# Kernel optimization log

Hardware: AMD Instinct MI355X
Metric: run time of the kernel (lower is better)

Reference implementation:

```python
import jax, jax.numpy as jnp
import numpy as np

NEG_SLOPE = 0.1  # LReLu_neg_slope
WEIGHT_INIT_STD = 1.0
N_GEN, N_LOAD, N_END = 25000, 25000, 25000
N_NODES = 100000
N_EDGES = 1600000
H = 128
N_HIDDEN_LAYERS = 3  # N_GCN_layers - 1


def _lin_w(key, n_in, n_out):
    # torch init: normal(std = weight_init_std / in_channels); stored as (in, out) for jax
    return jax.random.normal(key, (n_in, n_out), dtype=jnp.float32) * (WEIGHT_INIT_STD / n_in)


def setup_inputs() -> dict:
    key = jax.random.key(0)
    ks = jax.random.split(key, 24)
    inp = {
        "x_gen": jax.random.normal(ks[0], (N_GEN, 3), dtype=jnp.float32),
        "x_load": jax.random.normal(ks[1], (N_LOAD, 3), dtype=jnp.float32),
        "x_or": jax.random.normal(ks[2], (N_END, 6), dtype=jnp.float32),
        "x_ex": jax.random.normal(ks[3], (N_END, 6), dtype=jnp.float32),
        "edge_index": jax.random.randint(ks[4], (2, N_EDGES), 0, N_NODES, dtype=jnp.int64)
        if jax.config.jax_enable_x64 else jax.random.randint(ks[4], (2, N_EDGES), 0, N_NODES, dtype=jnp.int32),
        "object_ptv": jnp.arange(N_NODES, dtype=jnp.int32),
    }
    # per-type embedding MLPs (2 Linear layers each)
    inp["Wg1"], inp["bg1"] = _lin_w(ks[5], 3, H), jnp.zeros((H,), jnp.float32)
    inp["Wg2"], inp["bg2"] = _lin_w(ks[6], H, H), jnp.zeros((H,), jnp.float32)
    inp["Wld1"], inp["bld1"] = _lin_w(ks[7], 3, H), jnp.zeros((H,), jnp.float32)
    inp["Wld2"], inp["bld2"] = _lin_w(ks[8], H, H), jnp.zeros((H,), jnp.float32)
    inp["Wor1"], inp["bor1"] = _lin_w(ks[9], 6, H), jnp.zeros((H,), jnp.float32)
    inp["Wor2"], inp["bor2"] = _lin_w(ks[10], H, H), jnp.zeros((H,), jnp.float32)
    inp["Wex1"], inp["bex1"] = _lin_w(ks[11], 6, H), jnp.zeros((H,), jnp.float32)
    inp["Wex2"], inp["bex2"] = _lin_w(ks[12], H, H), jnp.zeros((H,), jnp.float32)
    # hidden SAGEConv layers (stacked): lin_l (neighbor, with bias) + lin_r (root, no bias)
    inp["Wl_h"] = jnp.stack([_lin_w(ks[13 + i], H, H) for i in range(N_HIDDEN_LAYERS)])
    inp["bl_h"] = jnp.zeros((N_HIDDEN_LAYERS, H), jnp.float32)
    inp["Wr_h"] = jnp.stack([_lin_w(ks[16 + i], H, H) for i in range(N_HIDDEN_LAYERS)])
    # output SAGEConv layer -> 1 unit
    inp["Wl_o"], inp["bl_o"] = _lin_w(ks[19], H, 1), jnp.zeros((1,), jnp.float32)
    inp["Wr_o"] = _lin_w(ks[20], H, 1)
    return inp


def _lrelu(x):
    return jax.nn.leaky_relu(x, NEG_SLOPE)


def _embed(x, W1, b1, W2, b2):
    return _lrelu(_lrelu(x @ W1 + b1) @ W2 + b2)


def reference(x_gen, x_load, x_or, x_ex, edge_index, object_ptv,
              Wg1, bg1, Wg2, bg2, Wld1, bld1, Wld2, bld2,
              Wor1, bor1, Wor2, bor2, Wex1, bex1, Wex2, bex2,
              Wl_h, bl_h, Wr_h, Wl_o, bl_o, Wr_o):
    x = jnp.concatenate([
        _embed(x_gen, Wg1, bg1, Wg2, bg2),
        _embed(x_load, Wld1, bld1, Wld2, bld2),
        _embed(x_or, Wor1, bor1, Wor2, bor2),
        _embed(x_ex, Wex1, bex1, Wex2, bex2),
    ], axis=0)
    x = x[object_ptv]                      # [N, H] in topology-vector order
    src, dst = edge_index[0], edge_index[1]
    n = x.shape[0]
    deg = jax.ops.segment_sum(jnp.ones_like(src, dtype=x.dtype), dst, num_segments=n)
    inv_deg = (1.0 / jnp.maximum(deg, 1.0))[:, None]

    def sage(h, Wl, bl, Wr):
        # SAGEConv(aggr='mean', root_weight=True): lin_l(mean_j h_j) + bias + lin_r(h_i)
        agg = jax.ops.segment_sum(h[src], dst, num_segments=n) * inv_deg
        return agg @ Wl + bl + h @ Wr

    for i in range(Wl_h.shape[0]):
        x = _lrelu(sage(x, Wl_h[i], bl_h[i], Wr_h[i]))
    return jax.nn.sigmoid(sage(x, Wl_o, bl_o, Wr_o))  # [N, 1]
```

## Files before the change

kernel.cpp:

```cpp
#include <hip/hip_runtime.h>
#include <hip/hip_bf16.h>
#include <hip/hip_fp16.h>
#include <math.h>

#define HD 128
#define NPB 512
#define CAP 16384
#define SCHUNK 4096
#define ALCSR 768

typedef __attribute__((ext_vector_type(8))) short  bf16x8;
typedef __attribute__((ext_vector_type(4))) float  f32x4;
typedef __attribute__((ext_vector_type(2))) _Float16 h16x2;

__device__ __forceinline__ float lrelu(float v) { return v > 0.0f ? v : 0.1f * v; }

__device__ __forceinline__ unsigned short f2bf(float f) {
  union { float f; unsigned u; } c; c.f = f;
  unsigned u = c.u + 0x7fffu + ((c.u >> 16) & 1u);
  return (unsigned short)(u >> 16);
}
__device__ __forceinline__ float bf2f(unsigned short u) {
  return __uint_as_float((unsigned)u << 16);
}
__device__ __forceinline__ unsigned char f2e5m2(float f) {
  unsigned short h = __half_as_ushort(__float2half(f));
  h = (unsigned short)(h + 0x7f + ((h >> 8) & 1));
  return (unsigned char)(h >> 8);
}

__global__ __launch_bounds__(256)
void embed1_kernel(const float* __restrict__ xg, const float* __restrict__ xl,
                   const float* __restrict__ xo, const float* __restrict__ xe,
                   const float* __restrict__ Wg, const float* __restrict__ bg,
                   const float* __restrict__ Wl, const float* __restrict__ bl,
                   const float* __restrict__ Wo, const float* __restrict__ bo,
                   const float* __restrict__ We, const float* __restrict__ be,
                   unsigned short* __restrict__ h1, int4 padCum, int4 realCnt) {
  int p = blockIdx.x * 2 + (threadIdx.x >> 7);
  if (p >= padCum.w) return;
  int j = threadIdx.x & 127;
  int typ = (p < padCum.x) ? 0 : (p < padCum.y) ? 1 : (p < padCum.z) ? 2 : 3;
  int padStart = (typ == 0) ? 0 : (typ == 1) ? padCum.x : (typ == 2) ? padCum.y : padCum.z;
  int cnt = (typ == 0) ? realCnt.x : (typ == 1) ? realCnt.y : (typ == 2) ? realCnt.z : realCnt.w;
  int loc = p - padStart;
  if (loc >= cnt) return;
  const float *x, *W, *bb; int IN;
  if (typ == 0)      { x = xg; W = Wg; bb = bg; IN = 3; }
  else if (typ == 1) { x = xl; W = Wl; bb = bl; IN = 3; }
  else if (typ == 2) { x = xo; W = Wo; bb = bo; IN = 6; }
  else               { x = xe; W = We; bb = be; IN = 6; }
  float acc = bb[j];
  for (int k = 0; k < IN; k++) acc += x[(size_t)loc * IN + k] * W[k * HD + j];
  h1[(size_t)p * HD + j] = f2bf(lrelu(acc));
}

__global__ __launch_bounds__(256)
void wprep_all_kernel(const float* __restrict__ Wg2, const float* __restrict__ Wld2,
                      const float* __restrict__ Wor2, const float* __restrict__ Wex2,
                      const float* __restrict__ Wl_h, const float* __restrict__ Wr_h,
                      unsigned short* __restrict__ Wp,
                      const int* __restrict__ ptv, int* __restrict__ inv,
                      int* __restrict__ gcnt, int n) {
  int tid = blockIdx.x * 256 + threadIdx.x;
  if (tid < 256) gcnt[tid] = 0;
  if (tid < n) inv[ptv[tid]] = tid;
  int m = tid >> 14;
  int i = tid & 16383;
  const float* src; unsigned short* dst;
  switch (m) {
    case 0: src = Wg2;  dst = Wp;             break;
    case 1: src = Wld2; dst = Wp + 16384;     break;
    case 2: src = Wor2; dst = Wp + 2 * 16384; break;
    case 3: src = Wex2; dst = Wp + 3 * 16384; break;
    default: {
      int mm = m - 4; int l = mm >> 1; int isR = mm & 1;
      src = (isR ? Wr_h : Wl_h) + (size_t)l * 16384;
      dst = Wp + 4 * 16384 + (size_t)l * 32768 + (isR ? 16384 : 0);
    }
  }
  int k = i >> 7, j = i & 127;
  int ks = k >> 5, g = (k >> 3) & 3, b = k & 7;
  dst[((ks * 128 + j) * 4 + g) * 8 + b] = f2bf(src[i]);
}

__global__ __launch_bounds__(256)
void mfma_embed2_kernel(const unsigned short* __restrict__ h1,
                        const unsigned short* __restrict__ Wp,
                        const float* __restrict__ b_g, const float* __restrict__ b_ld,
                        const float* __restrict__ b_or, const float* __restrict__ b_ex,
                        const int* __restrict__ inv, unsigned short* __restrict__ out,
                        int4 padCum, int4 realStart, int4 realCnt) {
  const int t = threadIdx.x, w = t >> 6, l = t & 63;
  const int lr = l & 15, lg = l >> 4;
  const int prow0 = blockIdx.x * 64 + w * 16;
  int typ = (prow0 < padCum.x) ? 0 : (prow0 < padCum.y) ? 1 : (prow0 < padCum.z) ? 2 : 3;
  int padStart = (typ == 0) ? 0 : (typ == 1) ? padCum.x : (typ == 2) ? padCum.y : padCum.z;
  int rStart = (typ == 0) ? realStart.x : (typ == 1) ? realStart.y : (typ == 2) ? realStart.z : realStart.w;
  int cnt = (typ == 0) ? realCnt.x : (typ == 1) ? realCnt.y : (typ == 2) ? realCnt.z : realCnt.w;
  const float* bias = (typ == 0) ? b_g : (typ == 1) ? b_ld : (typ == 2) ? b_or : b_ex;

  int raLoc = prow0 + lr - padStart; if (raLoc >= cnt) raLoc = cnt - 1;
  const unsigned short* abase = h1 + (size_t)(padStart + raLoc) * HD + 8 * lg;
  const unsigned short* wbase = Wp + (size_t)typ * 16384 + lr * 32 + lg * 8;

  f32x4 acc[8];
  #pragma unroll
  for (int cb = 0; cb < 8; cb++) {
    float bv = bias[cb * 16 + lr];
    acc[cb] = (f32x4){bv, bv, bv, bv};
  }
  #pragma unroll
  for (int ks = 0; ks < 4; ks++) {
    bf16x8 af = *(const bf16x8*)(abase + ks * 32);
    #pragma unroll
    for (int cb = 0; cb < 8; cb++) {
      bf16x8 bfv = *(const bf16x8*)(wbase + (size_t)(ks * 128 + cb * 16) * 32);
      acc[cb] = __builtin_amdgcn_mfma_f32_16x16x32_bf16(af, bfv, acc[cb], 0, 0, 0);
    }
  }
  int tgt[4];
  #pragma unroll
  for (int r = 0; r < 4; r++) {
    int locRow = prow0 + lg * 4 + r - padStart;
    tgt[r] = (locRow < cnt) ? inv[rStart + locRow] : -1;
  }
  #pragma unroll
  for (int cb = 0; cb < 8; cb++) {
    #pragma unroll
    for (int r = 0; r < 4; r++) {
      if (tgt[r] >= 0)
        out[(size_t)tgt[r] * HD + cb * 16 + lr] = f2bf(lrelu(acc[cb][r]));
    }
  }
}

__global__ __launch_bounds__(256)
void bf2f8_kernel(const unsigned short* __restrict__ in, unsigned char* __restrict__ out, int n8) {
  int idx = blockIdx.x * 256 + threadIdx.x;
  if (idx >= n8) return;
  uint4 v = *(const uint4*)(in + (size_t)idx * 8);
  unsigned char b0 = f2e5m2(__uint_as_float(v.x << 16));
  unsigned char b1 = f2e5m2(__uint_as_float(v.x & 0xffff0000u));
  unsigned char b2 = f2e5m2(__uint_as_float(v.y << 16));
  unsigned char b3 = f2e5m2(__uint_as_float(v.y & 0xffff0000u));
  unsigned char b4 = f2e5m2(__uint_as_float(v.z << 16));
  unsigned char b5 = f2e5m2(__uint_as_float(v.z & 0xffff0000u));
  unsigned char b6 = f2e5m2(__uint_as_float(v.w << 16));
  unsigned char b7 = f2e5m2(__uint_as_float(v.w & 0xffff0000u));
  uint2 o;
  o.x = (unsigned)b0 | ((unsigned)b1 << 8) | ((unsigned)b2 << 16) | ((unsigned)b3 << 24);
  o.y = (unsigned)b4 | ((unsigned)b5 << 8) | ((unsigned)b6 << 16) | ((unsigned)b7 << 24);
  *(uint2*)(out + (size_t)idx * 8) = o;
}

__global__ __launch_bounds__(256)
void bucket_scatter_kernel(const int* __restrict__ esrc, const int* __restrict__ edst,
                           int* __restrict__ gcnt, int* __restrict__ ebuf, int nE) {
  __shared__ int cnt[256];
  __shared__ int cur[256];
  const int t = threadIdx.x;
  const int c0 = blockIdx.x * SCHUNK;
  int s_arr[16], d_arr[16];
  cnt[t] = 0;
  __syncthreads();
  #pragma unroll
  for (int k = 0; k < 16; k++) {
    int idx = c0 + k * 256 + t;
    if (idx < nE) {
      s_arr[k] = esrc[idx];
      int d = edst[idx];
      d_arr[k] = d;
      atomicAdd(&cnt[d >> 9], 1);
    } else d_arr[k] = -1;
  }
  __syncthreads();
  if (cnt[t] > 0) cur[t] = atomicAdd(&gcnt[t], cnt[t]);
  __syncthreads();
  #pragma unroll
  for (int k = 0; k < 16; k++) {
    if (d_arr[k] >= 0) {
      int b = d_arr[k] >> 9;
      int p = atomicAdd(&cur[b], 1);
      ebuf[(size_t)b * CAP + p] = (s_arr[k] << 9) | (d_arr[k] & 511);
    }
  }
}

__device__ __forceinline__ int wave_incl_scan(int v) {
  int lane = threadIdx.x & 63;
  #pragma unroll
  for (int d = 1; d < 64; d <<= 1) {
    int tv = __shfl_up(v, d, 64);
    if (lane >= d) v += tv;
  }
  return v;
}

__global__ __launch_bounds__(256)
void bucket_build_kernel(const int* __restrict__ ebuf, const int* __restrict__ gcnt,
                         int* __restrict__ csr, int* __restrict__ offs,
                         int* __restrict__ deg, float* __restrict__ inv_deg, int n) {
  __shared__ int hist[512];
  __shared__ int offl[512];
  __shared__ int wsum[4];
  const int b = blockIdx.x, t = threadIdx.x;
  const int cnt = gcnt[b];
  const size_t ebase = (size_t)b * CAP;
  hist[t] = 0; hist[t + 256] = 0;
  __syncthreads();
  for (int i = t; i < cnt; i += 256) {
    int e = ebuf[ebase + i];
    atomicAdd(&hist[e & 511], 1);
  }
  __syncthreads();
  int a0 = hist[2 * t], a1 = hist[2 * t + 1];
  int s = a0 + a1;
  int incl = wave_incl_scan(s);
  int wid = t >> 6;
  if ((t & 63) == 63) wsum[wid] = incl;
  __syncthreads();
  int wbase = 0;
  for (int w_ = 0; w_ < wid; w_++) wbase += wsum[w_];
  int excl = wbase + incl - s;
  offl[2 * t] = excl;
  offl[2 * t + 1] = excl + a0;
  __syncthreads();
  const int d0 = b << 9;
  for (int i = t; i < 512; i += 256) {
    int g = d0 + i;
    if (g < n) {
      offs[g] = b * CAP + offl[i];
      int dg = hist[i];
      deg[g] = dg;
      inv_deg[g] = 1.0f / fmaxf((float)dg, 1.0f);
    }
  }
  __syncthreads();
  for (int i = t; i < cnt; i += 256) {
    int e = ebuf[ebase + i];
    int p = atomicAdd(&offl[e & 511], 1);
    csr[ebase + p] = ((unsigned)e) >> 9;
  }
}

template<bool EMIT_Z>
__global__ __launch_bounds__(256)
void sage_fused_kernel(const unsigned short* __restrict__ x, const unsigned char* __restrict__ xf8,
                       const int* __restrict__ csr,
                       const int* __restrict__ offs, const int* __restrict__ deg,
                       const float* __restrict__ inv_deg,
                       const unsigned short* __restrict__ Wp, const float* __restrict__ bias,
                       unsigned short* __restrict__ out, unsigned char* __restrict__ outf8,
                       const float* __restrict__ wl, const float* __restrict__ wr,
                       float* __restrict__ zl, float* __restrict__ zr, int n) {
  __shared__ int lcsr[ALCSR];
  __shared__ __align__(16) unsigned short lagg[16][136];
  __shared__ float zpart[2][4][16];
  const int t = threadIdx.x;
  const int node0 = blockIdx.x * 16;
  int last = node0 + 15; if (last >= n) last = n - 1;
  const int s_begin = offs[node0];
  const int total = offs[last] + deg[last] - s_begin;
  const bool useLds = (total <= ALCSR);
  if (useLds) {
    for (int k = t; k < total; k += 256) lcsr[k] = csr[s_begin + k];
  }
  __syncthreads();

  const int w = t >> 6, l = t & 63;
  {
    const int g = l >> 4, j = l & 15;
    const int node = node0 + w * 4 + g;
    if (node < n) {
      const unsigned char* xj = xf8 + 8 * j;
      const int lb = offs[node] - s_begin;
      const int d = deg[node];
      h16x2 a0[4], a1[4];
      #pragma unroll
      for (int k = 0; k < 4; k++) {
        a0[k] = (h16x2){(_Float16)0, (_Float16)0};
        a1[k] = (h16x2){(_Float16)0, (_Float16)0};
      }
      auto acc8 = [](h16x2* A, uint2 v) {
        unsigned p0 = __builtin_amdgcn_perm(0u, v.x, 0x01040004u);
        unsigned p1 = __builtin_amdgcn_perm(0u, v.x, 0x03040204u);
        unsigned p2 = __builtin_amdgcn_perm(0u, v.y, 0x01040004u);
        unsigned p3 = __builtin_amdgcn_perm(0u, v.y, 0x03040204u);
        A[0] += __builtin_bit_cast(h16x2, p0);
        A[1] += __builtin_bit_cast(h16x2, p1);
        A[2] += __builtin_bit_cast(h16x2, p2);
        A[3] += __builtin_bit_cast(h16x2, p3);
      };
      int i = 0;
      if (useLds) {
        for (; i + 3 < d; i += 4) {
          int e0 = lcsr[lb + i], e1 = lcsr[lb + i + 1];
          int e2 = lcsr[lb + i + 2], e3 = lcsr[lb + i + 3];
          uint2 v0 = *(const uint2*)(xj + (size_t)e0 * HD);
          uint2 v1 = *(const uint2*)(xj + (size_t)e1 * HD);
          uint2 v2 = *(const uint2*)(xj + (size_t)e2 * HD);
          uint2 v3 = *(const uint2*)(xj + (size_t)e3 * HD);
          acc8(a0, v0); acc8(a1, v1); acc8(a0, v2); acc8(a1, v3);
        }
        if (i + 1 < d) {
          int e0 = lcsr[lb + i], e1 = lcsr[lb + i + 1];
          uint2 v0 = *(const uint2*)(xj + (size_t)e0 * HD);
          uint2 v1 = *(const uint2*)(xj + (size_t)e1 * HD);
          acc8(a0, v0); acc8(a1, v1);
          i += 2;
        }
        if (i < d) {
          int e0 = lcsr[lb + i];
          acc8(a0, *(const uint2*)(xj + (size_t)e0 * HD));
        }
      } else {
        const int* gcsr = csr + s_begin + lb;
        for (; i + 3 < d; i += 4) {
          int e0 = gcsr[i], e1 = gcsr[i + 1], e2 = gcsr[i + 2], e3 = gcsr[i + 3];
          uint2 v0 = *(const uint2*)(xj + (size_t)e0 * HD);
          uint2 v1 = *(const uint2*)(xj + (size_t)e1 * HD);
          uint2 v2 = *(const uint2*)(xj + (size_t)e2 * HD);
          uint2 v3 = *(const uint2*)(xj + (size_t)e3 * HD);
          acc8(a0, v0); acc8(a1, v1); acc8(a0, v2); acc8(a1, v3);
        }
        if (i + 1 < d) {
          int e0 = gcsr[i], e1 = gcsr[i + 1];
          uint2 v0 = *(const uint2*)(xj + (size_t)e0 * HD);
          uint2 v1 = *(const uint2*)(xj + (size_t)e1 * HD);
          acc8(a0, v0); acc8(a1, v1);
          i += 2;
        }
        if (i < d) {
          int e0 = gcsr[i];
          acc8(a0, *(const uint2*)(xj + (size_t)e0 * HD));
        }
      }
      const float id = inv_deg[node];
      uint4 o;
      unsigned* op = (unsigned*)&o;
      #pragma unroll
      for (int k = 0; k < 4; k++) {
        float lo = ((float)a0[k][0] + (float)a1[k][0]) * id;
        float hi = ((float)a0[k][1] + (float)a1[k][1]) * id;
        op[k] = (unsigned)f2bf(lo) | ((unsigned)f2bf(hi) << 16);
      }
      *(uint4*)&lagg[w * 4 + g][j * 8] = o;
    } else {
      *(uint4*)&lagg[w * 4 + g][j * 8] = make_uint4(0, 0, 0, 0);
    }
  }
  __syncthreads();

  const int lr = l & 15, lg = l >> 4;
  int ra = node0 + lr; if (ra >= n) ra = n - 1;
  const unsigned short* wbase = Wp + (size_t)lr * 32 + (size_t)lg * 8;
  const unsigned short* rbase = x + (size_t)ra * HD + 8 * lg;

  f32x4 acc[2];
  #pragma unroll
  for (int c = 0; c < 2; c++) {
    float bv = bias[(2 * w + c) * 16 + lr];
    acc[c] = (f32x4){bv, bv, bv, bv};
  }
  #pragma unroll
  for (int ks = 0; ks < 4; ks++) {
    bf16x8 af = *(const bf16x8*)&lagg[lr][lg * 8 + ks * 32];
    #pragma unroll
    for (int c = 0; c < 2; c++) {
      int cb = 2 * w + c;
      bf16x8 bfv = *(const bf16x8*)(wbase + (size_t)(ks * 128 + cb * 16) * 32);
      acc[c] = __builtin_amdgcn_mfma_f32_16x16x32_bf16(af, bfv, acc[c], 0, 0, 0);
    }
  }
  #pragma unroll
  for (int ks = 0; ks < 4; ks++) {
    bf16x8 af = *(const bf16x8*)(rbase + ks * 32);
    #pragma unroll
    for (int c = 0; c < 2; c++) {
      int cb = 2 * w + c;
      bf16x8 bfv = *(const bf16x8*)(wbase + (size_t)((4 + ks) * 128 + cb * 16) * 32);
      acc[c] = __builtin_amdgcn_mfma_f32_16x16x32_bf16(af, bfv, acc[c], 0, 0, 0);
    }
  }

  if constexpr (!EMIT_Z) {
    #pragma unroll
    for (int c = 0; c < 2; c++) {
      int cb = 2 * w + c;
      #pragma unroll
      for (int r = 0; r < 4; r++) {
        int node = node0 + lg * 4 + r;
        if (node < n) {
          float val = lrelu(acc[c][r]);
          out[(size_t)node * HD + cb * 16 + lr] = f2bf(val);
          outf8[(size_t)node * HD + cb * 16 + lr] = f2e5m2(val);
        }
      }
    }
  } else {
    float vl[4] = {0.f, 0.f, 0.f, 0.f}, vr[4] = {0.f, 0.f, 0.f, 0.f};
    #pragma unroll
    for (int c = 0; c < 2; c++) {
      int cb = 2 * w + c;
      float wlv = wl[cb * 16 + lr];
      float wrv = wr[cb * 16 + lr];
      #pragma unroll
      for (int r = 0; r < 4; r++) {
        float x3 = lrelu(acc[c][r]);
        vl[r] += x3 * wlv;
        vr[r] += x3 * wrv;
      }
    }
    #pragma unroll
    for (int r = 0; r < 4; r++) {
      #pragma unroll
      for (int d = 1; d < 16; d <<= 1) {
        vl[r] += __shfl_xor(vl[r], d, 64);
        vr[r] += __shfl_xor(vr[r], d, 64);
      }
    }
    if (lr == 0) {
      #pragma unroll
      for (int r = 0; r < 4; r++) {
        zpart[0][w][lg * 4 + r] = vl[r];
        zpart[1][w][lg * 4 + r] = vr[r];
      }
    }
    __syncthreads();
    if (t < 16) {
      int node = node0 + t;
      if (node < n) {
        zl[node] = zpart[0][0][t] + zpart[0][1][t] + zpart[0][2][t] + zpart[0][3][t];
        zr[node] = zpart[1][0][t] + zpart[1][1][t] + zpart[1][2][t] + zpart[1][3][t];
      }
    }
  }
}

__global__ __launch_bounds__(256)
void zfinal_kernel(const float* __restrict__ zl, const float* __restrict__ zr,
                   const int* __restrict__ csr, const int* __restrict__ offs,
                   const int* __restrict__ deg, const float* __restrict__ inv_deg,
                   const float* __restrict__ bl, float* __restrict__ out, int n) {
  int i = blockIdx.x * 256 + threadIdx.x;
  if (i >= n) return;
  int s0 = offs[i], d = deg[i];
  float a = 0.f;
  #pragma unroll 4
  for (int e = 0; e < d; e++) a += zl[csr[s0 + e]];
  float s = a * inv_deg[i] + bl[0] + zr[i];
  out[i] = 1.0f / (1.0f + expf(-s));
}

extern "C" void kernel_launch(void* const* d_in, const int* in_sizes, int n_in,
                              void* d_out, int out_size, void* d_ws, size_t ws_size,
                              hipStream_t stream) {
  const float* x_gen  = (const float*)d_in[0];
  const float* x_load = (const float*)d_in[1];
  const float* x_or   = (const float*)d_in[2];
  const float* x_ex   = (const float*)d_in[3];
  const int*   edge   = (const int*)d_in[4];
  const int*   ptv    = (const int*)d_in[5];
  const float* Wg1  = (const float*)d_in[6],  *bg1  = (const float*)d_in[7];
  const float* Wg2  = (const float*)d_in[8],  *bg2  = (const float*)d_in[9];
  const float* Wld1 = (const float*)d_in[10], *bld1 = (const float*)d_in[11];
  const float* Wld2 = (const float*)d_in[12], *bld2 = (const float*)d_in[13];
  const float* Wor1 = (const float*)d_in[14], *bor1 = (const float*)d_in[15];
  const float* Wor2 = (const float*)d_in[16], *bor2 = (const float*)d_in[17];
  const float* Wex1 = (const float*)d_in[18], *bex1 = (const float*)d_in[19];
  const float* Wex2 = (const float*)d_in[20], *bex2 = (const float*)d_in[21];
  const float* Wl_h = (const float*)d_in[22], *bl_h = (const float*)d_in[23];
  const float* Wr_h = (const float*)d_in[24];
  const float* Wl_o = (const float*)d_in[25], *bl_o = (const float*)d_in[26];
  const float* Wr_o = (const float*)d_in[27];

  const int n_gen  = in_sizes[0] / 3;
  const int n_load = in_sizes[1] / 3;
  const int n_or   = in_sizes[2] / 6;
  const int n_ex   = in_sizes[3] / 6;
  const int nE     = in_sizes[4] / 2;
  const int N      = in_sizes[5];
  const int* esrc = edge;
  const int* edst = edge + nE;

  const int np0 = ((n_gen  + 63) / 64) * 64;
  const int np1 = ((n_load + 63) / 64) * 64;
  const int np2 = ((n_or   + 63) / 64) * 64;
  const int np3 = ((n_ex   + 63) / 64) * 64;
  const int NP  = np0 + np1 + np2 + np3;
  const int4 padCum    = make_int4(np0, np0 + np1, np0 + np1 + np2, NP);
  const int4 realStart = make_int4(0, n_gen, n_gen + n_load, n_gen + n_load + n_or);
  const int4 realCnt   = make_int4(n_gen, n_load, n_or, n_ex);

  const int NB = (N + NPB - 1) / NPB;

  size_t NPel = (size_t)NP * HD;
  size_t nel  = (size_t)N * HD;
  unsigned short* b0 = (unsigned short*)d_ws;
  unsigned short* b1 = b0 + NPel;
  unsigned short* b3 = b1 + nel;
  int*  gcnt = (int*)(b3 + nel);
  int*  ebuf = gcnt + 256;
  int*  csr  = ebuf + (size_t)NB * CAP;
  int*  offs = csr + (size_t)NB * CAP;
  int*  deg  = offs + N;
  float* inv_deg = (float*)(deg + N);
  float* zl = inv_deg + N;
  float* zr = zl + N;
  int*  invp = (int*)(zr + N);
  uintptr_t wp_addr = ((uintptr_t)(invp + N) + 15) & ~(uintptr_t)15;
  unsigned short* Wp = (unsigned short*)wp_addr;
  uintptr_t f8_addr = ((uintptr_t)(Wp + 4 * 16384 + 3 * 32768) + 15) & ~(uintptr_t)15;
  unsigned char* f8a = (unsigned char*)f8_addr;
  unsigned char* f8b = f8a + nel;

  wprep_all_kernel<<<640, 256, 0, stream>>>(Wg2, Wld2, Wor2, Wex2, Wl_h, Wr_h, Wp,
                                            ptv, invp, gcnt, N);

  embed1_kernel<<<NP / 2, 256, 0, stream>>>(x_gen, x_load, x_or, x_ex,
                                            Wg1, bg1, Wld1, bld1, Wor1, bor1, Wex1, bex1,
                                            b0, padCum, realCnt);
  mfma_embed2_kernel<<<NP / 64, 256, 0, stream>>>(b0, Wp, bg2, bld2, bor2, bex2,
                                                  invp, b1, padCum, realStart, realCnt);
  bf2f8_kernel<<<(N * 16 + 255) / 256, 256, 0, stream>>>(b1, f8a, N * 16);

  bucket_scatter_kernel<<<(nE + SCHUNK - 1) / SCHUNK, 256, 0, stream>>>(esrc, edst, gcnt, ebuf, nE);
  bucket_build_kernel<<<NB, 256, 0, stream>>>(ebuf, gcnt, csr, offs, deg, inv_deg, N);

  const int fGrid = (N + 15) / 16;
  const unsigned short* WpC = Wp + 4 * 16384;
  unsigned short* xbf = b1;  unsigned char* xf8 = f8a;
  unsigned short* nbf = b3;  unsigned char* nf8 = f8b;
  for (int l = 0; l < 2; l++) {
    sage_fused_kernel<false><<<fGrid, 256, 0, stream>>>(
        xbf, xf8, csr, offs, deg, inv_deg, WpC + (size_t)l * 32768,
        bl_h + (size_t)l * HD, nbf, nf8, nullptr, nullptr, nullptr, nullptr, N);
    unsigned short* tb = xbf; xbf = nbf; nbf = tb;
    unsigned char*  tf = xf8; xf8 = nf8; nf8 = tf;
  }
  sage_fused_kernel<true><<<fGrid, 256, 0, stream>>>(
      xbf, xf8, csr, offs, deg, inv_deg, WpC + 2 * 32768,
      bl_h + 2 * HD, nullptr, nullptr, Wl_o, Wr_o, zl, zr, N);

  zfinal_kernel<<<(N + 255) / 256, 256, 0, stream>>>(zl, zr, csr, offs, deg, inv_deg,
                                                     bl_o, (float*)d_out, N);
}
```

Baseline: 319.6 us.

## Fuse fp8 conversion into embed epilogue and stage CSR build through LDS

The embed GEMM epilogue now writes the e5m2 copy directly, which removes the separate bf16-to-fp8 kernel and its extra pass over the activations. The bucket scatter first sorts each chunk's edges locally in shared memory, then writes them out contiguously per bucket, so global stores coalesce better. The CSR build permutes edges in an LDS buffer and writes the CSR sequentially when the bucket fits, falling back to global scatter otherwise. The costs are larger shared-memory footprints, which may reduce occupancy, and a binary search per element during the scatter write-out.

```diff
diff --git a/kernel.cpp b/kernel.cpp
--- a/kernel.cpp
+++ b/kernel.cpp
@@ -8,6 +8,7 @@
 #define CAP 16384
 #define SCHUNK 4096
 #define ALCSR 768
+#define LCAP 9216
 
 typedef __attribute__((ext_vector_type(8))) short  bf16x8;
 typedef __attribute__((ext_vector_type(4))) float  f32x4;
@@ -90,6 +91,7 @@
                         const float* __restrict__ b_g, const float* __restrict__ b_ld,
                         const float* __restrict__ b_or, const float* __restrict__ b_ex,
                         const int* __restrict__ inv, unsigned short* __restrict__ out,
+                        unsigned char* __restrict__ outf8,
                         int4 padCum, int4 realStart, int4 realCnt) {
   const int t = threadIdx.x, w = t >> 6, l = t & 63;
   const int lr = l & 15, lg = l >> 4;
@@ -129,36 +131,34 @@
   for (int cb = 0; cb < 8; cb++) {
     #pragma unroll
     for (int r = 0; r < 4; r++) {
-      if (tgt[r] >= 0)
-        out[(size_t)tgt[r] * HD + cb * 16 + lr] = f2bf(lrelu(acc[cb][r]));
-    }
-  }
-}
-
-__global__ __launch_bounds__(256)
-void bf2f8_kernel(const unsigned short* __restrict__ in, unsigned char* __restrict__ out, int n8) {
-  int idx = blockIdx.x * 256 + threadIdx.x;
-  if (idx >= n8) return;
-  uint4 v = *(const uint4*)(in + (size_t)idx * 8);
-  unsigned char b0 = f2e5m2(__uint_as_float(v.x << 16));
-  unsigned char b1 = f2e5m2(__uint_as_float(v.x & 0xffff0000u));
-  unsigned char b2 = f2e5m2(__uint_as_float(v.y << 16));
-  unsigned char b3 = f2e5m2(__uint_as_float(v.y & 0xffff0000u));
-  unsigned char b4 = f2e5m2(__uint_as_float(v.z << 16));
-  unsigned char b5 = f2e5m2(__uint_as_float(v.z & 0xffff0000u));
-  unsigned char b6 = f2e5m2(__uint_as_float(v.w << 16));
-  unsigned char b7 = f2e5m2(__uint_as_float(v.w & 0xffff0000u));
-  uint2 o;
-  o.x = (unsigned)b0 | ((unsigned)b1 << 8) | ((unsigned)b2 << 16) | ((unsigned)b3 << 24);
-  o.y = (unsigned)b4 | ((unsigned)b5 << 8) | ((unsigned)b6 << 16) | ((unsigned)b7 << 24);
-  *(uint2*)(out + (size_t)idx * 8) = o;
+      if (tgt[r] >= 0) {
+        float val = lrelu(acc[cb][r]);
+        out[(size_t)tgt[r] * HD + cb * 16 + lr] = f2bf(val);
+        outf8[(size_t)tgt[r] * HD + cb * 16 + lr] = f2e5m2(val);
+      }
+    }
+  }
+}
+
+__device__ __forceinline__ int wave_incl_scan(int v) {
+  int lane = threadIdx.x & 63;
+  #pragma unroll
+  for (int d = 1; d < 64; d <<= 1) {
+    int tv = __shfl_up(v, d, 64);
+    if (lane >= d) v += tv;
+  }
+  return v;
 }
 
 __global__ __launch_bounds__(256)
 void bucket_scatter_kernel(const int* __restrict__ esrc, const int* __restrict__ edst,
                            int* __restrict__ gcnt, int* __restrict__ ebuf, int nE) {
   __shared__ int cnt[256];
+  __shared__ int loff[257];
+  __shared__ int gbase[256];
   __shared__ int cur[256];
+  __shared__ int wsum[4];
+  __shared__ int sbuf[SCHUNK];
   const int t = threadIdx.x;
   const int c0 = blockIdx.x * SCHUNK;
   int s_arr[16], d_arr[16];
@@ -175,26 +175,37 @@
     } else d_arr[k] = -1;
   }
   __syncthreads();
-  if (cnt[t] > 0) cur[t] = atomicAdd(&gcnt[t], cnt[t]);
+  int v = cnt[t];
+  int incl = wave_incl_scan(v);
+  int wid = t >> 6;
+  if ((t & 63) == 63) wsum[wid] = incl;
+  if (v > 0) gbase[t] = atomicAdd(&gcnt[t], v);
+  __syncthreads();
+  int add = 0;
+  for (int w_ = 0; w_ < wid; w_++) add += wsum[w_];
+  int excl = add + incl - v;
+  loff[t] = excl;
+  cur[t] = excl;
+  if (t == 255) loff[256] = excl + v;
   __syncthreads();
   #pragma unroll
   for (int k = 0; k < 16; k++) {
     if (d_arr[k] >= 0) {
       int b = d_arr[k] >> 9;
       int p = atomicAdd(&cur[b], 1);
-      ebuf[(size_t)b * CAP + p] = (s_arr[k] << 9) | (d_arr[k] & 511);
-    }
-  }
-}
-
-__device__ __forceinline__ int wave_incl_scan(int v) {
-  int lane = threadIdx.x & 63;
-  #pragma unroll
-  for (int d = 1; d < 64; d <<= 1) {
-    int tv = __shfl_up(v, d, 64);
-    if (lane >= d) v += tv;
-  }
-  return v;
+      sbuf[p] = (s_arr[k] << 9) | (d_arr[k] & 511);
+    }
+  }
+  __syncthreads();
+  const int totalc = loff[256];
+  for (int k = t; k < totalc; k += 256) {
+    int lo = 0, hi = 255;
+    while (lo < hi) {
+      int mid = (lo + hi + 1) >> 1;
+      if (loff[mid] <= k) lo = mid; else hi = mid - 1;
+    }
+    ebuf[(size_t)lo * CAP + gbase[lo] + (k - loff[lo])] = sbuf[k];
+  }
 }
 
 __global__ __launch_bounds__(256)
@@ -203,7 +214,9 @@
                          int* __restrict__ deg, float* __restrict__ inv_deg, int n) {
   __shared__ int hist[512];
   __shared__ int offl[512];
+  __shared__ int curl[512];
   __shared__ int wsum[4];
+  __shared__ int lbuf[LCAP];
   const int b = blockIdx.x, t = threadIdx.x;
   const int cnt = gcnt[b];
   const size_t ebase = (size_t)b * CAP;
@@ -220,11 +233,11 @@
   int wid = t >> 6;
   if ((t & 63) == 63) wsum[wid] = incl;
   __syncthreads();
-  int wbase = 0;
-  for (int w_ = 0; w_ < wid; w_++) wbase += wsum[w_];
-  int excl = wbase + incl - s;
-  offl[2 * t] = excl;
-  offl[2 * t + 1] = excl + a0;
+  int add = 0;
+  for (int w_ = 0; w_ < wid; w_++) add += wsum[w_];
+  int excl = add + incl - s;
+  offl[2 * t] = excl;     offl[2 * t + 1] = excl + a0;
+  curl[2 * t] = excl;     curl[2 * t + 1] = excl + a0;
   __syncthreads();
   const int d0 = b << 9;
   for (int i = t; i < 512; i += 256) {
@@ -237,10 +250,20 @@
     }
   }
   __syncthreads();
-  for (int i = t; i < cnt; i += 256) {
-    int e = ebuf[ebase + i];
-    int p = atomicAdd(&offl[e & 511], 1);
-    csr[ebase + p] = ((unsigned)e) >> 9;
+  if (cnt <= LCAP) {
+    for (int i = t; i < cnt; i += 256) {
+      int e = ebuf[ebase + i];
+      int p = atomicAdd(&curl[e & 511], 1);
+      lbuf[p] = ((unsigned)e) >> 9;
+    }
+    __syncthreads();
+    for (int i = t; i < cnt; i += 256) csr[ebase + i] = lbuf[i];
+  } else {
+    for (int i = t; i < cnt; i += 256) {
+      int e = ebuf[ebase + i];
+      int p = atomicAdd(&curl[e & 511], 1);
+      csr[ebase + p] = ((unsigned)e) >> 9;
+    }
   }
 }
 
@@ -522,8 +545,7 @@
                                             Wg1, bg1, Wld1, bld1, Wor1, bor1, Wex1, bex1,
                                             b0, padCum, realCnt);
   mfma_embed2_kernel<<<NP / 64, 256, 0, stream>>>(b0, Wp, bg2, bld2, bor2, bex2,
-                                                  invp, b1, padCum, realStart, realCnt);
-  bf2f8_kernel<<<(N * 16 + 255) / 256, 256, 0, stream>>>(b1, f8a, N * 16);
+                                                  invp, b1, f8a, padCum, realStart, realCnt);
 
   bucket_scatter_kernel<<<(nE + SCHUNK - 1) / SCHUNK, 256, 0, stream>>>(esrc, edst, gcnt, ebuf, nE);
   bucket_build_kernel<<<NB, 256, 0, stream>>>(ebuf, gcnt, csr, offs, deg, inv_deg, N);
```

Result: no change. 315.1 us (-1.4%).
